# Kernel optimization log

Hardware: AMD Instinct MI355X
Metric: run time of the kernel (lower is better)

Reference implementation:

```python
import jax, jax.numpy as jnp
import numpy as np
from jax import lax

GAMMA_FLOW = 0.001
GAMMA_MASK = 0.0005
INTERP_RATIOS = (0.5,)


def setup_inputs() -> dict:
    key = jax.random.key(0)
    k1, k2, k3 = jax.random.split(key, 3)
    N, H, W, Ce = 8, 512, 512, 32
    frames = jax.random.uniform(k1, (N, H, W, 6), dtype=jnp.float32)
    encoded = jax.random.normal(k2, (N, H, W, Ce), dtype=jnp.float32)
    # small init so tanh is not saturated, like a trained conv head
    conv_w = jax.random.normal(k3, (3, 3, Ce, 3), dtype=jnp.float32) * 0.05
    conv_b = jnp.zeros((3,), dtype=jnp.float32)
    return {"frames": frames, "encoded": encoded, "conv_w": conv_w, "conv_b": conv_b}


def _total_variation(x):
    # matches tf.image.total_variation summed over the batch
    return (jnp.sum(jnp.abs(x[:, 1:] - x[:, :-1])) +
            jnp.sum(jnp.abs(x[:, :, 1:] - x[:, :, :-1])))


def _bilinear_interp(image, new_hh, new_ww):
    # image: [N,H,W,C]; new_hh/new_ww: [N,H,W] normalized coords in [-1,1]
    N, H, W, C = image.shape
    hh = (new_hh + 1.0) * (H - 1) / 2.0
    ww = (new_ww + 1.0) * (W - 1) / 2.0
    h0 = jnp.floor(hh).astype(jnp.int32)
    w0 = jnp.floor(ww).astype(jnp.int32)
    h1 = jnp.clip(h0 + 1, 0, H - 1)
    w1 = jnp.clip(w0 + 1, 0, W - 1)
    h0 = jnp.clip(h0, 0, H - 1)
    w0 = jnp.clip(w0, 0, W - 1)
    img_flat = image.reshape(N, H * W, C)

    def gather(h, w):
        idx = (h * W + w).reshape(N, H * W, 1)
        return jnp.take_along_axis(img_flat, idx, axis=1).reshape(N, H, W, C)

    ru = gather(h0, w0)
    rd = gather(h1, w0)
    lu = gather(h0, w1)
    ld = gather(h1, w1)
    h1f = h1.astype(hh.dtype)
    w1f = w1.astype(ww.dtype)
    w_ru = ((h1f - hh) * (w1f - ww))[..., None]
    w_rd = ((1.0 - (h1f - hh)) * (w1f - ww))[..., None]
    w_lu = ((h1f - hh) * (1.0 - (w1f - ww)))[..., None]
    w_ld = ((1.0 - (h1f - hh)) * (1.0 - (w1f - ww)))[..., None]
    return w_ru * ru + w_rd * rd + w_lu * lu + w_ld * ld


def reference(frames, encoded, conv_w, conv_b):
    frame0 = frames[..., 0:3]
    frame1 = frames[..., 3:6]
    N, H, W, _ = frame0.shape
    # 3x3 SAME conv + tanh (the layer's float32 conv head)
    net = jnp.tanh(
        lax.conv_general_dilated(encoded, conv_w, (1, 1), 'SAME',
                                 dimension_numbers=('NHWC', 'HWIO', 'NHWC'))
        + conv_b)
    flow = net[..., 0:2]

    hh = jnp.broadcast_to(jnp.linspace(-1.0, 1.0, H)[None, :, None], (N, H, W))
    ww = jnp.broadcast_to(jnp.linspace(-1.0, 1.0, W)[None, None, :], (N, H, W))

    total_pixels = float(N * H * W * 3)
    tv_loss = GAMMA_FLOW * _total_variation(flow) / total_pixels

    output_frames = []
    for i, alpha in enumerate(INTERP_RATIOS):
        mask = net[..., i + 2:i + 3]
        tv_loss = tv_loss + GAMMA_MASK * _total_variation(mask) / total_pixels
        coor_h_0 = hh + flow[..., 0] * alpha
        coor_w_0 = ww + flow[..., 1] * alpha
        coor_h_1 = hh - flow[..., 0] * (1.0 - alpha)
        coor_w_1 = ww - flow[..., 1] * (1.0 - alpha)
        out0 = _bilinear_interp(frame0, coor_h_0, coor_w_0)
        out1 = _bilinear_interp(frame1, coor_h_1, coor_w_1)
        m = 0.5 * (1.0 + mask)
        output_frames.append(m * out0 + (1.0 - m) * out1)
    stacked = jnp.concatenate(output_frames, axis=-1)
    return stacked, flow, tv_loss
```

## Files before the change

### kernel.cpp

```cpp
#include <hip/hip_runtime.h>
#include <hip/hip_fp16.h>
#include <math.h>

#define HH 512
#define WW 512
#define NIMG 8
#define NPIX (NIMG * HH * WW)
#define GAMMA_FLOW 0.001f
#define GAMMA_MASK 0.0005f
#define INV_TOTAL (1.0f / (float)(NPIX * 3))

#define CVT_BLOCKS  (NPIX / 256)
#define CONV_BLOCKS (NPIX / 128)
#define FAT_BLOCKS  (CVT_BLOCKS + CONV_BLOCKS)

__device__ __forceinline__ float tanh_fast(float x)
{
    float e = __expf(2.0f * x);
    return 1.0f - 2.0f / (e + 1.0f);
}

__device__ __forceinline__ float2 pk_fma(float2 a, float2 b, float2 c)
{
    float2 d;
    asm("v_pk_fma_f32 %0, %1, %2, %3" : "=v"(d) : "v"(a), "v"(b), "v"(c));
    return d;
}

__global__ __launch_bounds__(256, 4) void fat_kernel(
    const float* __restrict__ enc, const float* __restrict__ cw,
    const float* __restrict__ cb, const float* __restrict__ frames,
    float* __restrict__ flow, float* __restrict__ mask,
    __half* __restrict__ f0h, __half* __restrict__ f1h,
    float* __restrict__ tv_out)
{
    __shared__ float wlds[864];

    int bid = blockIdx.x;

    if (bid % 3 == 0) {
        int ci = bid / 3;
        int t  = ci * 256 + threadIdx.x;
        if (t == 0) tv_out[0] = 0.0f;
        const float2* fp = reinterpret_cast<const float2*>(frames + (size_t)t * 6);
        float2 v0 = fp[0], v1 = fp[1], v2 = fp[2];
        __half2 a = __floats2half2_rn(v0.x, v0.y);
        __half2 b = __floats2half2_rn(v1.x, 0.0f);
        __half2 c = __floats2half2_rn(v1.y, v2.x);
        __half2 d = __floats2half2_rn(v2.y, 0.0f);
        __half2* p0 = reinterpret_cast<__half2*>(f0h) + (size_t)t * 2;
        __half2* p1 = reinterpret_cast<__half2*>(f1h) + (size_t)t * 2;
        p0[0] = a; p0[1] = b;
        p1[0] = c; p1[1] = d;
        return;
    }

    int ci  = bid - (bid + 2) / 3;
    int wb  = (ci & 7) * (CONV_BLOCKS / 8) + (ci >> 3);
    int px0 = wb * 128;
    int n = px0 >> 18;
    int h = (px0 >> 9) & (HH - 1);

    int tid  = threadIdx.x;

    for (int e = tid; e < 864; e += 256) {
        int t = e / 96;
        int r = e - t * 96;
        int o = r >> 5;
        int c = r & 31;
        wlds[e] = cw[(t * 32 + c) * 3 + o];
    }
    __syncthreads();

    int wv   = tid >> 6;
    int lane = tid & 63;
    int pg   = lane >> 3;
    int c4   = lane & 7;

    int wbase = (px0 & (WW - 1)) + wv * 32;
    int pxb   = wbase + pg * 4;

    const float* imgbase = enc + ((size_t)n * HH) * (WW * 32);
    const float* wbase_lds = &wlds[c4 * 4];

    float2 pacc[4][3];
#pragma unroll
    for (int p = 0; p < 4; ++p)
#pragma unroll
        for (int o = 0; o < 3; ++o)
            pacc[p][o] = make_float2(0.f, 0.f);

    bool edge = (wbase == 0) || (wbase == WW - 32);

#pragma unroll
    for (int kh = 0; kh < 3; ++kh) {
        int hr = h + kh - 1;
        if ((unsigned)hr >= (unsigned)HH) continue;
        const float* rowp = imgbase + (size_t)hr * (WW * 32);

        float4 win[6];
        if (!edge) {
            const float* pB = rowp + (pxb - 1) * 32 + c4 * 4;
#pragma unroll
            for (int j = 0; j < 6; ++j)
                win[j] = *reinterpret_cast<const float4*>(pB + j * 32);
        } else {
#pragma unroll
            for (int j = 0; j < 6; ++j) {
                int col = pxb + j - 1;
                win[j] = make_float4(0.f, 0.f, 0.f, 0.f);
                if ((unsigned)col < (unsigned)WW)
                    win[j] = *reinterpret_cast<const float4*>(
                                 rowp + (size_t)col * 32 + c4 * 4);
            }
        }

#pragma unroll
        for (int kw = 0; kw < 3; ++kw) {
            int t = kh * 3 + kw;
#pragma unroll
            for (int o = 0; o < 3; ++o) {
                float4 w4 = *reinterpret_cast<const float4*>(
                                wbase_lds + t * 96 + o * 32);
                float2 wlo = make_float2(w4.x, w4.y);
                float2 whi = make_float2(w4.z, w4.w);
#pragma unroll
                for (int p = 0; p < 4; ++p) {
                    float2 xlo = make_float2(win[p + kw].x, win[p + kw].y);
                    float2 xhi = make_float2(win[p + kw].z, win[p + kw].w);
                    pacc[p][o] = pk_fma(xlo, wlo, pacc[p][o]);
                    pacc[p][o] = pk_fma(xhi, whi, pacc[p][o]);
                }
            }
        }
    }

    float b0 = cb[0], b1 = cb[1], b2 = cb[2];
    size_t rowidx = ((size_t)n * HH + h) * WW;

    float acc[4][3];
#pragma unroll
    for (int p = 0; p < 4; ++p) {
#pragma unroll
        for (int o = 0; o < 3; ++o)
            acc[p][o] = pacc[p][o].x + pacc[p][o].y;
#pragma unroll
        for (int off = 1; off < 8; off <<= 1) {
            acc[p][0] += __shfl_xor(acc[p][0], off);
            acc[p][1] += __shfl_xor(acc[p][1], off);
            acc[p][2] += __shfl_xor(acc[p][2], off);
        }
    }
    if (c4 == 0) {
#pragma unroll
        for (int p = 0; p < 4; ++p) {
            size_t idx = rowidx + (size_t)(pxb + p);
            *reinterpret_cast<float2*>(flow + idx * 2) =
                make_float2(tanh_fast(acc[p][0] + b0),
                            tanh_fast(acc[p][1] + b1));
            mask[idx] = tanh_fast(acc[p][2] + b2);
        }
    }
}

__device__ __forceinline__ void bilerp_h(const __half* __restrict__ img,
                                         float ch, float cwv, float out[3])
{
    float hp = (ch + 1.0f) * 255.5f;
    float wp = (cwv + 1.0f) * 255.5f;
    int h0 = (int)floorf(hp);
    int w0 = (int)floorf(wp);
    int h1  = min(max(h0 + 1, 0), HH - 1);
    int w1  = min(max(w0 + 1, 0), WW - 1);
    int h0c = min(max(h0, 0), HH - 1);
    int w0c = min(max(w0, 0), WW - 1);
    float wh = (float)h1 - hp;
    float wv = (float)w1 - wp;
    float w_ru = wh * wv;
    float w_rd = (1.0f - wh) * wv;
    float w_lu = wh * (1.0f - wv);
    float w_ld = (1.0f - wh) * (1.0f - wv);

    int q = min(w0c, WW - 2);
    bool Ahi = (w0c != q);
    bool Bhi = (w1 == q + 1);
    float4 U = *reinterpret_cast<const float4*>(img + (size_t)(((h0c << 9) + q) << 2));
    float4 D = *reinterpret_cast<const float4*>(img + (size_t)(((h1  << 9) + q) << 2));
    float ru_ab = Ahi ? U.z : U.x, ru_c = Ahi ? U.w : U.y;
    float rd_ab = Ahi ? D.z : D.x, rd_c = Ahi ? D.w : D.y;
    float lu_ab = Bhi ? U.z : U.x, lu_c = Bhi ? U.w : U.y;
    float ld_ab = Bhi ? D.z : D.x, ld_c = Bhi ? D.w : D.y;

    float2 ruA = __half22float2(*reinterpret_cast<__half2*>(&ru_ab));
    float2 rdA = __half22float2(*reinterpret_cast<__half2*>(&rd_ab));
    float2 luA = __half22float2(*reinterpret_cast<__half2*>(&lu_ab));
    float2 ldA = __half22float2(*reinterpret_cast<__half2*>(&ld_ab));
    float ruZ = __half2float(reinterpret_cast<__half2*>(&ru_c)->x);
    float rdZ = __half2float(reinterpret_cast<__half2*>(&rd_c)->x);
    float luZ = __half2float(reinterpret_cast<__half2*>(&lu_c)->x);
    float ldZ = __half2float(reinterpret_cast<__half2*>(&ld_c)->x);

    out[0] = w_ru * ruA.x + w_rd * rdA.x + w_lu * luA.x + w_ld * ldA.x;
    out[1] = w_ru * ruA.y + w_rd * rdA.y + w_lu * luA.y + w_ld * ldA.y;
    out[2] = w_ru * ruZ   + w_rd * rdZ   + w_lu * luZ   + w_ld * ldZ;
}

__global__ __launch_bounds__(256, 4) void interp_tv_kernel(
    const __half* __restrict__ f0h, const __half* __restrict__ f1h,
    const float* __restrict__ flow, const float* __restrict__ mask,
    float* __restrict__ stacked, float* __restrict__ tv_out)
{
    int bid = blockIdx.x;
    int wb  = (bid & 7) * (NPIX / 2048 / 8) + (bid >> 3);
    int idx0 = wb * 2048 + (int)threadIdx.x * 8;
    int w0 = idx0 & (WW - 1);
    int h  = (idx0 >> 9) & (HH - 1);
    int n  = idx0 >> 18;

    float4 fl[4];
#pragma unroll
    for (int j = 0; j < 4; ++j)
        fl[j] = *reinterpret_cast<const float4*>(flow + (size_t)idx0 * 2 + j * 4);
    float4 mkA = *reinterpret_cast<const float4*>(mask + idx0);
    float4 mkB = *reinterpret_cast<const float4*>(mask + idx0 + 4);
    const float* flp = reinterpret_cast<const float*>(fl);
    float mkp[8] = {mkA.x, mkA.y, mkA.z, mkA.w, mkB.x, mkB.y, mkB.z, mkB.w};

    float hhv = -1.0f + (float)h * (2.0f / 511.0f);

    const __half* i0 = f0h + (size_t)n * (HH * WW * 4);
    const __half* i1 = f1h + (size_t)n * (HH * WW * 4);

    float res[24];
#pragma unroll
    for (int p = 0; p < 8; ++p) {
        float wvx = -1.0f + (float)(w0 + p) * (2.0f / 511.0f);
        float fx = flp[p * 2], fy = flp[p * 2 + 1];
        float o0[3], o1[3];
        bilerp_h(i0, hhv + fx * 0.5f, wvx + fy * 0.5f, o0);
        bilerp_h(i1, hhv - fx * 0.5f, wvx - fy * 0.5f, o1);
        float m = 0.5f * (1.0f + mkp[p]), om = 1.0f - m;
#pragma unroll
        for (int c = 0; c < 3; ++c)
            res[p * 3 + c] = m * o0[c] + om * o1[c];
    }
    float4* sp = reinterpret_cast<float4*>(stacked + (size_t)idx0 * 3);
#pragma unroll
    for (int j = 0; j < 6; ++j)
        sp[j] = make_float4(res[j * 4], res[j * 4 + 1],
                            res[j * 4 + 2], res[j * 4 + 3]);

    float tvf = 0.0f, tvm = 0.0f;
#pragma unroll
    for (int p = 0; p < 7; ++p) {
        tvf += fabsf(flp[p * 2 + 2] - flp[p * 2])
             + fabsf(flp[p * 2 + 3] - flp[p * 2 + 1]);
        tvm += fabsf(mkp[p + 1] - mkp[p]);
    }
    if (w0 < WW - 8) {
        float2 flr = *reinterpret_cast<const float2*>(flow + (size_t)(idx0 + 8) * 2);
        float  mkr = mask[idx0 + 8];
        tvf += fabsf(flr.x - flp[14]) + fabsf(flr.y - flp[15]);
        tvm += fabsf(mkr - mkp[7]);
    }
    if (h < HH - 1) {
#pragma unroll
        for (int j = 0; j < 4; ++j) {
            float4 fd = *reinterpret_cast<const float4*>(
                            flow + (size_t)(idx0 + WW) * 2 + j * 4);
            tvf += fabsf(fd.x - flp[j * 4 + 0]) + fabsf(fd.y - flp[j * 4 + 1])
                 + fabsf(fd.z - flp[j * 4 + 2]) + fabsf(fd.w - flp[j * 4 + 3]);
        }
        float4 mdA = *reinterpret_cast<const float4*>(mask + idx0 + WW);
        float4 mdB = *reinterpret_cast<const float4*>(mask + idx0 + WW + 4);
        tvm += fabsf(mdA.x - mkp[0]) + fabsf(mdA.y - mkp[1])
             + fabsf(mdA.z - mkp[2]) + fabsf(mdA.w - mkp[3])
             + fabsf(mdB.x - mkp[4]) + fabsf(mdB.y - mkp[5])
             + fabsf(mdB.z - mkp[6]) + fabsf(mdB.w - mkp[7]);
    }
    float tv = GAMMA_FLOW * tvf + GAMMA_MASK * tvm;
#pragma unroll
    for (int off = 32; off > 0; off >>= 1) tv += __shfl_xor(tv, off);
    if ((threadIdx.x & 63) == 0) atomicAdd(tv_out, tv * INV_TOTAL);
}

extern "C" void kernel_launch(void* const* d_in, const int* in_sizes, int n_in,
                              void* d_out, int out_size, void* d_ws, size_t ws_size,
                              hipStream_t stream)
{
    const float* frames  = (const float*)d_in[0];
    const float* encoded = (const float*)d_in[1];
    const float* conv_w  = (const float*)d_in[2];
    const float* conv_b  = (const float*)d_in[3];

    float* out     = (float*)d_out;
    float* stacked = out;
    float* flow    = out + (size_t)NPIX * 3;
    float* tv      = out + (size_t)NPIX * 5;

    const size_t frame_bytes = (size_t)NPIX * 4 * sizeof(__half);
    __half* f0h = (__half*)d_ws;
    __half* f1h = (__half*)((char*)d_ws + frame_bytes);
    float*  mask = (float*)((char*)d_ws + 2 * frame_bytes);

    fat_kernel<<<FAT_BLOCKS, 256, 0, stream>>>(
        encoded, conv_w, conv_b, frames, flow, mask, f0h, f1h, tv);
    interp_tv_kernel<<<NPIX / 2048, 256, 0, stream>>>(
        f0h, f1h, flow, mask, stacked, tv);
}
```

Baseline: 198.4 us.

## Split conv across fused convert kernel and separate prefetching conv kernel

The fused kernel now interleaves frame-conversion blocks with conv blocks covering only the first half of the pixels, with an even 1:1 block mix. A new convB kernel handles the second half of the conv. Its interior path software-pipelines the three input rows, loading the next row while FMAs on the current row run. This adds a kernel launch and duplicates code, and the extra window registers may lower occupancy.

```diff
diff --git a/kernel.cpp b/kernel.cpp
--- a/kernel.cpp
+++ b/kernel.cpp
@@ -10,9 +10,11 @@
 #define GAMMA_MASK 0.0005f
 #define INV_TOTAL (1.0f / (float)(NPIX * 3))
 
-#define CVT_BLOCKS  (NPIX / 256)
-#define CONV_BLOCKS (NPIX / 128)
-#define FAT_BLOCKS  (CVT_BLOCKS + CONV_BLOCKS)
+#define HALF_PIX     (NPIX / 2)
+#define CVT_BLOCKS   (NPIX / 256)
+#define CONVA_BLOCKS (HALF_PIX / 128)
+#define FAT_BLOCKS   (CVT_BLOCKS + CONVA_BLOCKS)
+#define CONVB_BLOCKS (HALF_PIX / 128)
 
 __device__ __forceinline__ float tanh_fast(float x)
 {
@@ -37,9 +39,11 @@
     __shared__ float wlds[864];
 
     int bid = blockIdx.x;
-
-    if (bid % 3 == 0) {
-        int ci = bid / 3;
+    int k   = bid >> 4;
+    int r   = bid & 15;
+
+    if (r < 8) {
+        int ci = k * 8 + r;
         int t  = ci * 256 + threadIdx.x;
         if (t == 0) tv_out[0] = 0.0f;
         const float2* fp = reinterpret_cast<const float2*>(frames + (size_t)t * 6);
@@ -55,22 +59,20 @@
         return;
     }
 
-    int ci  = bid - (bid + 2) / 3;
-    int wb  = (ci & 7) * (CONV_BLOCKS / 8) + (ci >> 3);
+    int ci  = k * 8 + (r - 8);
+    int tid = threadIdx.x;
+
+    for (int e = tid; e < 864; e += 256) {
+        int t = e / 96;
+        int rr = e - t * 96;
+        wlds[e] = cw[(t * 32 + (rr & 31)) * 3 + (rr >> 5)];
+    }
+    __syncthreads();
+
+    int wb  = (ci & 7) * (CONVA_BLOCKS / 8) + (ci >> 3);
     int px0 = wb * 128;
     int n = px0 >> 18;
     int h = (px0 >> 9) & (HH - 1);
-
-    int tid  = threadIdx.x;
-
-    for (int e = tid; e < 864; e += 256) {
-        int t = e / 96;
-        int r = e - t * 96;
-        int o = r >> 5;
-        int c = r & 31;
-        wlds[e] = cw[(t * 32 + c) * 3 + o];
-    }
-    __syncthreads();
 
     int wv   = tid >> 6;
     int lane = tid & 63;
@@ -81,7 +83,7 @@
     int pxb   = wbase + pg * 4;
 
     const float* imgbase = enc + ((size_t)n * HH) * (WW * 32);
-    const float* wbase_lds = &wlds[c4 * 4];
+    const float* wlp = &wlds[c4 * 4];
 
     float2 pacc[4][3];
 #pragma unroll
@@ -121,7 +123,7 @@
 #pragma unroll
             for (int o = 0; o < 3; ++o) {
                 float4 w4 = *reinterpret_cast<const float4*>(
-                                wbase_lds + t * 96 + o * 32);
+                                wlp + t * 96 + o * 32);
                 float2 wlo = make_float2(w4.x, w4.y);
                 float2 whi = make_float2(w4.z, w4.w);
 #pragma unroll
@@ -132,6 +134,132 @@
                     pacc[p][o] = pk_fma(xhi, whi, pacc[p][o]);
                 }
             }
+        }
+    }
+
+    float b0 = cb[0], b1 = cb[1], b2 = cb[2];
+    size_t rowidx = ((size_t)n * HH + h) * WW;
+
+    float acc[4][3];
+#pragma unroll
+    for (int p = 0; p < 4; ++p) {
+#pragma unroll
+        for (int o = 0; o < 3; ++o)
+            acc[p][o] = pacc[p][o].x + pacc[p][o].y;
+#pragma unroll
+        for (int off = 1; off < 8; off <<= 1) {
+            acc[p][0] += __shfl_xor(acc[p][0], off);
+            acc[p][1] += __shfl_xor(acc[p][1], off);
+            acc[p][2] += __shfl_xor(acc[p][2], off);
+        }
+    }
+    if (c4 == 0) {
+#pragma unroll
+        for (int p = 0; p < 4; ++p) {
+            size_t idx = rowidx + (size_t)(pxb + p);
+            *reinterpret_cast<float2*>(flow + idx * 2) =
+                make_float2(tanh_fast(acc[p][0] + b0),
+                            tanh_fast(acc[p][1] + b1));
+            mask[idx] = tanh_fast(acc[p][2] + b2);
+        }
+    }
+}
+
+__global__ __launch_bounds__(256, 3) void convB_kernel(
+    const float* __restrict__ enc, const float* __restrict__ cw,
+    const float* __restrict__ cb, float* __restrict__ flow,
+    float* __restrict__ mask)
+{
+    __shared__ float wlds[864];
+
+    int tid = threadIdx.x;
+    for (int e = tid; e < 864; e += 256) {
+        int t = e / 96;
+        int rr = e - t * 96;
+        wlds[e] = cw[(t * 32 + (rr & 31)) * 3 + (rr >> 5)];
+    }
+    __syncthreads();
+
+    int bid = blockIdx.x;
+    int wb  = (bid & 7) * (CONVB_BLOCKS / 8) + (bid >> 3);
+    int px0 = HALF_PIX + wb * 128;
+    int n = px0 >> 18;
+    int h = (px0 >> 9) & (HH - 1);
+
+    int wv   = tid >> 6;
+    int lane = tid & 63;
+    int pg   = lane >> 3;
+    int c4   = lane & 7;
+
+    int wbase = (px0 & (WW - 1)) + wv * 32;
+    int pxb   = wbase + pg * 4;
+
+    const float* imgbase = enc + ((size_t)n * HH) * (WW * 32);
+    const float* wlp = &wlds[c4 * 4];
+
+    float2 pacc[4][3];
+#pragma unroll
+    for (int p = 0; p < 4; ++p)
+#pragma unroll
+        for (int o = 0; o < 3; ++o)
+            pacc[p][o] = make_float2(0.f, 0.f);
+
+    bool edge = (wbase == 0) || (wbase == WW - 32);
+    bool interior = (h > 0) && (h < HH - 1) && !edge;
+
+    auto fma_row = [&](int kh, const float4* win) {
+#pragma unroll
+        for (int kw = 0; kw < 3; ++kw) {
+            int t = kh * 3 + kw;
+#pragma unroll
+            for (int o = 0; o < 3; ++o) {
+                float4 w4 = *reinterpret_cast<const float4*>(
+                                wlp + t * 96 + o * 32);
+                float2 wlo = make_float2(w4.x, w4.y);
+                float2 whi = make_float2(w4.z, w4.w);
+#pragma unroll
+                for (int p = 0; p < 4; ++p) {
+                    float2 xlo = make_float2(win[p + kw].x, win[p + kw].y);
+                    float2 xhi = make_float2(win[p + kw].z, win[p + kw].w);
+                    pacc[p][o] = pk_fma(xlo, wlo, pacc[p][o]);
+                    pacc[p][o] = pk_fma(xhi, whi, pacc[p][o]);
+                }
+            }
+        }
+    };
+
+    if (interior) {
+        const float* r0 = imgbase + (size_t)(h - 1) * (WW * 32)
+                        + (pxb - 1) * 32 + c4 * 4;
+        float4 winA[6], winB[6];
+#pragma unroll
+        for (int j = 0; j < 6; ++j)
+            winA[j] = *reinterpret_cast<const float4*>(r0 + j * 32);
+#pragma unroll
+        for (int j = 0; j < 6; ++j)
+            winB[j] = *reinterpret_cast<const float4*>(r0 + WW * 32 + j * 32);
+        fma_row(0, winA);
+#pragma unroll
+        for (int j = 0; j < 6; ++j)
+            winA[j] = *reinterpret_cast<const float4*>(r0 + 2 * WW * 32 + j * 32);
+        fma_row(1, winB);
+        fma_row(2, winA);
+    } else {
+#pragma unroll
+        for (int kh = 0; kh < 3; ++kh) {
+            int hr = h + kh - 1;
+            if ((unsigned)hr >= (unsigned)HH) continue;
+            const float* rowp = imgbase + (size_t)hr * (WW * 32);
+            float4 win[6];
+#pragma unroll
+            for (int j = 0; j < 6; ++j) {
+                int col = pxb + j - 1;
+                win[j] = make_float4(0.f, 0.f, 0.f, 0.f);
+                if ((unsigned)col < (unsigned)WW)
+                    win[j] = *reinterpret_cast<const float4*>(
+                                 rowp + (size_t)col * 32 + c4 * 4);
+            }
+            fma_row(kh, win);
         }
     }
 
@@ -305,6 +433,8 @@
 
     fat_kernel<<<FAT_BLOCKS, 256, 0, stream>>>(
         encoded, conv_w, conv_b, frames, flow, mask, f0h, f1h, tv);
+    convB_kernel<<<CONVB_BLOCKS, 256, 0, stream>>>(
+        encoded, conv_w, conv_b, flow, mask);
     interp_tv_kernel<<<NPIX / 2048, 256, 0, stream>>>(
         f0h, f1h, flow, mask, stacked, tv);
 }
```

After: 259.0 us. 30.5% more time.
